# Performance work log

Measured on AMD Instinct MI355X. Metric: run time of the kernel, lower is better.

Reference implementation:

```python
import jax, jax.numpy as jnp
import numpy as np

MODEL_DIM = 1024
NUM_HEADS = 16
HEAD_DIM = MODEL_DIM // NUM_HEADS  # 64
MAX_SEQ = 1024
MAX_REL = 8


def setup_inputs() -> dict:
    key = jax.random.key(0)
    ks = jax.random.split(key, 5)
    B, S = 4, 1024
    x = jax.random.normal(ks[0], (B, S, MODEL_DIM), jnp.float32)
    W_in = jax.random.normal(ks[1], (MODEL_DIM, MODEL_DIM), jnp.float32) * 0.02
    W_out = jax.random.normal(ks[2], (MODEL_DIM, MODEL_DIM), jnp.float32) * 0.02
    # learned synthesized attention scores [1, H, max_seq, max_seq]
    attn_scores = jax.random.normal(ks[3], (1, NUM_HEADS, MAX_SEQ, MAX_SEQ), jnp.float32) * 0.05
    # relative-position VALUE embedding table [2*max_rel+1, head_dim]
    rel_values = jax.random.normal(ks[4], (2 * MAX_REL + 1, HEAD_DIM), jnp.float32) * 0.02
    return {"x": x, "W_in": W_in, "W_out": W_out,
            "attn_scores": attn_scores, "rel_values": rel_values}


def reference(x, W_in, W_out, attn_scores, rel_values):
    B, S, D = x.shape
    H, hd = NUM_HEADS, HEAD_DIM
    # in-projection (no bias), split heads: [B, H, S, hd]
    value = (x @ W_in.T).reshape(B, S, H, hd).transpose(0, 2, 1, 3)
    # learned (random-synthesizer) scores, sliced to seq len, broadcast over batch
    scores = attn_scores[:, :, :S, :S]              # [1, H, S, S]
    probs = jax.nn.softmax(scores, axis=-1)          # [1, H, S, S]
    probs = jnp.broadcast_to(probs, (B, H, S, S))
    # attention output: probs @ V
    out = jnp.einsum('bhsj,bhjd->bhsd', probs, value)  # [B, H, S, hd]
    # relative-position value contribution
    r = jnp.arange(S)
    dist = r[None, :] - r[:, None]                   # [S, S]
    idx = jnp.clip(dist, -MAX_REL, MAX_REL) + MAX_REL
    rel_emb = rel_values[idx]                        # [S, S, hd]
    out = out + jnp.einsum('bhsj,sjd->bhsd', probs, rel_emb)
    # join heads and out-project
    out = out.transpose(0, 2, 1, 3).reshape(B, S, H * hd)
    return out @ W_out.T                             # [B, S, D]
```

## Files before the change

kernel.cpp:

```cpp
#include <hip/hip_runtime.h>

typedef unsigned short ushort_t;
typedef __attribute__((ext_vector_type(4))) short short4_t;
typedef __attribute__((ext_vector_type(8))) short short8;
typedef __attribute__((ext_vector_type(4))) float floatx4;
typedef __attribute__((ext_vector_type(8))) __bf16 bf16x8;

__device__ __forceinline__ ushort_t f2b(float f) {
  union { float f; unsigned int i; } t; t.f = f;
  unsigned int u = t.i;
  return (ushort_t)((u + 0x7fffu + ((u >> 16) & 1u)) >> 16);
}

__device__ __forceinline__ floatx4 mfma16(short8 a, short8 b, floatx4 c) {
  return __builtin_amdgcn_mfma_f32_16x16x32_bf16(
      __builtin_bit_cast(bf16x8, a), __builtin_bit_cast(bf16x8, b), c, 0, 0, 0);
}

__device__ __forceinline__ void gload16(const void* g, void* l) {
  __builtin_amdgcn_global_load_lds(
      (const __attribute__((address_space(1))) void*)g,
      (__attribute__((address_space(3))) void*)l, 16, 0, 0);
}

__global__ __launch_bounds__(256) void k_f2b_all(
    const float* __restrict__ x, const float* __restrict__ Wi,
    const float* __restrict__ Wo, ushort_t* __restrict__ xb,
    ushort_t* __restrict__ Wib, ushort_t* __restrict__ Wob)
{
  const float* in; ushort_t* out; int i;
  if (blockIdx.x < 2048)      { in = x;  out = xb;  i = (blockIdx.x * 256 + threadIdx.x) * 8; }
  else if (blockIdx.x < 2560) { in = Wi; out = Wib; i = ((blockIdx.x - 2048) * 256 + threadIdx.x) * 8; }
  else                        { in = Wo; out = Wob; i = ((blockIdx.x - 2560) * 256 + threadIdx.x) * 8; }
  float4 a = *reinterpret_cast<const float4*>(in + i);
  float4 b = *reinterpret_cast<const float4*>(in + i + 4);
  short8 o;
  o[0] = (short)f2b(a.x); o[1] = (short)f2b(a.y);
  o[2] = (short)f2b(a.z); o[3] = (short)f2b(a.w);
  o[4] = (short)f2b(b.x); o[5] = (short)f2b(b.y);
  o[6] = (short)f2b(b.z); o[7] = (short)f2b(b.w);
  *reinterpret_cast<short8*>(out + i) = o;
}

__global__ __launch_bounds__(256) void k_softmax_rel(
    const float* __restrict__ S, const float* __restrict__ relv,
    ushort_t* __restrict__ P, float* __restrict__ R)
{
  __shared__ float mid[4][16];
  const int wave = threadIdx.x >> 6, lane = threadIdx.x & 63;
  const int row = blockIdx.x * 4 + wave;
  const int s = row & 1023;
  const float* src = S + (size_t)row * 1024;

  float v[4][4];
#pragma unroll
  for (int c = 0; c < 4; ++c) {
    float4 raw = *reinterpret_cast<const float4*>(src + c * 256 + lane * 4);
    v[c][0] = raw.x; v[c][1] = raw.y; v[c][2] = raw.z; v[c][3] = raw.w;
  }
  float m = -1e30f;
#pragma unroll
  for (int c = 0; c < 4; ++c)
#pragma unroll
    for (int e = 0; e < 4; ++e) m = fmaxf(m, v[c][e]);
#pragma unroll
  for (int d = 32; d; d >>= 1) m = fmaxf(m, __shfl_xor(m, d));

  float p[4][4];
  float tot = 0.f, sA = 0.f, sB = 0.f;
#pragma unroll
  for (int c = 0; c < 4; ++c) {
#pragma unroll
    for (int e = 0; e < 4; ++e) {
      int j = c * 256 + lane * 4 + e;
      float pe = __expf(v[c][e] - m);
      p[c][e] = pe;
      tot += pe;
      sA += (j <= s - 8) ? pe : 0.f;
      sB += (j >= s + 8) ? pe : 0.f;
    }
  }
#pragma unroll
  for (int d = 32; d; d >>= 1) {
    tot += __shfl_xor(tot, d);
    sA  += __shfl_xor(sA, d);
    sB  += __shfl_xor(sB, d);
  }
  const float inv = 1.0f / tot;

  if (lane < 16) mid[wave][lane] = 0.f;
  __syncthreads();
#pragma unroll
  for (int c = 0; c < 4; ++c) {
#pragma unroll
    for (int e = 0; e < 4; ++e) {
      int j = c * 256 + lane * 4 + e;
      int tt = j - (s - 7);
      if (tt >= 0 && tt < 15) mid[wave][tt] = p[c][e];
    }
  }
  __syncthreads();

  float acc = sA * relv[lane] + sB * relv[16 * 64 + lane];
#pragma unroll
  for (int tt = 0; tt < 15; ++tt)
    acc += mid[wave][tt] * relv[(1 + tt) * 64 + lane];
  R[(size_t)row * 64 + lane] = acc * inv;

#pragma unroll
  for (int c = 0; c < 4; ++c) {
    short4_t o;
#pragma unroll
    for (int e = 0; e < 4; ++e) o[e] = (short)f2b(p[c][e] * inv);
    *reinterpret_cast<short4_t*>(P + (size_t)row * 1024 + c * 256 + lane * 4) = o;
  }
}

__device__ __forceinline__ void gemm128_loop(
    const ushort_t* __restrict__ A0, const ushort_t* __restrict__ B0,
    ushort_t* sA, ushort_t* sB, floatx4 (&acc)[4][2])
{
  const int t = threadIdx.x;
  const int lane = t & 63, wave = t >> 6;
  const int wm = wave & 1, wn = wave >> 1;
  const int l15 = lane & 15, lk = lane >> 4;

#define STG(kt, buf)                                                        \
  {                                                                         \
    const int k0 = (kt) << 6;                                               \
    _Pragma("unroll")                                                       \
    for (int cc = 0; cc < 2; ++cc) {                                        \
      int c = t + (cc << 9);                                                \
      int r = c >> 3, cb = c & 7;                                           \
      int sc = k0 + ((cb ^ (r & 7)) << 3);                                  \
      gload16(A0 + (size_t)r * 1024 + sc, (char*)sA + (buf) * 16384 + c * 16); \
      gload16(B0 + (size_t)r * 1024 + sc, (char*)sB + (buf) * 16384 + c * 16); \
    }                                                                       \
  }

  STG(0, 0);
  STG(1, 1);
  for (int kt = 0; kt < 16; ++kt) {
    if (kt < 14) {
      STG(kt + 2, (kt + 2) & 3);
      asm volatile("s_waitcnt vmcnt(8)" ::: "memory");
    } else if (kt == 14) {
      asm volatile("s_waitcnt vmcnt(4)" ::: "memory");
    } else {
      asm volatile("s_waitcnt vmcnt(0)" ::: "memory");
    }
    __builtin_amdgcn_s_barrier();
    const char* bA = (const char*)sA + (kt & 3) * 16384;
    const char* bB = (const char*)sB + (kt & 3) * 16384;
#pragma unroll
    for (int kk = 0; kk < 2; ++kk) {
      const int cs = (kk << 2) + lk;
      short8 af[4], bf[2];
#pragma unroll
      for (int i = 0; i < 4; ++i) {
        int ra = (wm << 6) + (i << 4) + l15;
        af[i] = *reinterpret_cast<const short8*>(
            bA + ra * 128 + ((cs ^ (ra & 7)) << 4));
      }
#pragma unroll
      for (int j = 0; j < 2; ++j) {
        int rb = (wn << 5) + (j << 4) + l15;
        bf[j] = *reinterpret_cast<const short8*>(
            bB + rb * 128 + ((cs ^ (rb & 7)) << 4));
      }
      __builtin_amdgcn_s_setprio(1);
#pragma unroll
      for (int i = 0; i < 4; ++i)
#pragma unroll
        for (int j = 0; j < 2; ++j)
          acc[i][j] = mfma16(af[i], bf[j], acc[i][j]);
      __builtin_amdgcn_s_setprio(0);
    }
  }
#undef STG
}

__device__ __forceinline__ int xcd_swz(int bid) {
  return ((bid & 7) << 5) | (bid >> 3);
}

__global__ __launch_bounds__(512) void k_gemm_xw(
    const ushort_t* __restrict__ W, const ushort_t* __restrict__ X,
    ushort_t* __restrict__ Yt)
{
  __shared__ ushort_t sA[4 * 128 * 64];
  __shared__ ushort_t sB[4 * 128 * 64];
  const int lg = xcd_swz(blockIdx.x);
  const int m0 = (lg & 7) << 7, n0 = (lg >> 3) << 7;
  floatx4 acc[4][2] = {};
  gemm128_loop(W + (size_t)m0 * 1024, X + (size_t)n0 * 1024, sA, sB, acc);

  const int lane = threadIdx.x & 63, wave = threadIdx.x >> 6;
  const int wm = wave & 1, wn = wave >> 1;
  const int l15 = lane & 15, lk = lane >> 4;
#pragma unroll
  for (int i = 0; i < 4; ++i)
#pragma unroll
    for (int j = 0; j < 2; ++j)
#pragma unroll
      for (int rr = 0; rr < 4; ++rr) {
        int wrow = m0 + (wm << 6) + (i << 4) + (lk << 2) + rr;
        int col  = n0 + (wn << 5) + (j << 4) + l15;
        int h = wrow >> 6, d = wrow & 63;
        int b = col >> 10, s = col & 1023;
        Yt[(((size_t)((h << 2) + b) << 6) + d) * 1024 + s] = f2b(acc[i][j][rr]);
      }
}

__global__ __launch_bounds__(512) void k_head_pv(
    const ushort_t* __restrict__ P, const ushort_t* __restrict__ Yt,
    const float* __restrict__ R, ushort_t* __restrict__ O)
{
  __shared__ ushort_t sA[4 * 128 * 64];
  __shared__ ushort_t sB[4 * 128 * 64];
  const int lg = xcd_swz(blockIdx.x);
  const int h = lg >> 4, rem = lg & 15;
  const int m0 = (rem >> 1) << 7, n0 = (rem & 1) << 7;
  floatx4 acc[4][2] = {};
  gemm128_loop(P + ((size_t)h << 20) + (size_t)m0 * 1024,
               Yt + ((size_t)h << 18) + (size_t)n0 * 1024, sA, sB, acc);

  const int lane = threadIdx.x & 63, wave = threadIdx.x >> 6;
  const int wm = wave & 1, wn = wave >> 1;
  const int l15 = lane & 15, lk = lane >> 4;
#pragma unroll
  for (int i = 0; i < 4; ++i)
#pragma unroll
    for (int j = 0; j < 2; ++j)
#pragma unroll
      for (int rr = 0; rr < 4; ++rr) {
        int sr = m0 + (wm << 6) + (i << 4) + (lk << 2) + rr;
        int c  = n0 + (wn << 5) + (j << 4) + l15;
        int b = c >> 6, d = c & 63;
        float val = acc[i][j][rr] + R[(((size_t)h << 10) + sr) * 64 + d];
        O[((size_t)b << 20) + ((size_t)sr << 10) + (h << 6) + d] = f2b(val);
      }
}

__global__ __launch_bounds__(512) void k_gemm_out(
    const ushort_t* __restrict__ A, const ushort_t* __restrict__ B,
    float* __restrict__ C)
{
  __shared__ ushort_t sA[4 * 128 * 64];
  __shared__ ushort_t sB[4 * 128 * 64];
  const int lg = xcd_swz(blockIdx.x);
  const int m0 = (lg >> 3) << 7, n0 = (lg & 7) << 7;
  floatx4 acc[4][2] = {};
  gemm128_loop(A + (size_t)m0 * 1024, B + (size_t)n0 * 1024, sA, sB, acc);

  const int lane = threadIdx.x & 63, wave = threadIdx.x >> 6;
  const int wm = wave & 1, wn = wave >> 1;
  const int l15 = lane & 15, lk = lane >> 4;
#pragma unroll
  for (int i = 0; i < 4; ++i)
#pragma unroll
    for (int j = 0; j < 2; ++j)
#pragma unroll
      for (int rr = 0; rr < 4; ++rr) {
        int rowg = m0 + (wm << 6) + (i << 4) + (lk << 2) + rr;
        int colg = n0 + (wn << 5) + (j << 4) + l15;
        C[(size_t)rowg * 1024 + colg] = acc[i][j][rr];
      }
}

extern "C" void kernel_launch(void* const* d_in, const int* in_sizes, int n_in,
                              void* d_out, int out_size, void* d_ws, size_t ws_size,
                              hipStream_t stream)
{
  const float* x     = (const float*)d_in[0];
  const float* W_in  = (const float*)d_in[1];
  const float* W_out = (const float*)d_in[2];
  const float* attn  = (const float*)d_in[3];
  const float* relv  = (const float*)d_in[4];
  float* out = (float*)d_out;

  char* ws = (char*)d_ws;
  ushort_t* xb  = (ushort_t*)(ws);
  ushort_t* Wib = (ushort_t*)(ws + (8u << 20));
  ushort_t* Wob = (ushort_t*)(ws + (10u << 20));
  ushort_t* P   = (ushort_t*)(ws + (12u << 20));
  float*    R   = (float*)   (ws + (44u << 20));
  ushort_t* Yt  = (ushort_t*)(ws + (48u << 20));
  ushort_t* O   = (ushort_t*)(ws + (56u << 20));

  k_f2b_all<<<3072, 256, 0, stream>>>(x, W_in, W_out, xb, Wib, Wob);
  k_softmax_rel<<<4096, 256, 0, stream>>>(attn, relv, P, R);
  k_gemm_xw<<<256, 512, 0, stream>>>(Wib, xb, Yt);
  k_head_pv<<<256, 512, 0, stream>>>(P, Yt, R, O);
  k_gemm_out<<<256, 512, 0, stream>>>(O, Wob, out);
}
```

Before: 66.92 us.

## Merge softmax-rel and input-projection GEMM into one heterogeneous launch

Combines the independent softmax/relative-value kernel and the x·W_in GEMM into a single launch. The first 256 blocks do the GEMM and the remaining 2048 blocks each process 8 softmax rows, so the memory-bound softmax can overlap with the compute-bound GEMM and one launch is removed. To fit the shared 64KB buffer, the GEMM in this fused kernel drops from a 4-stage to a 2-stage, syncthreads-based pipeline, which may expose more load latency. The softmax blocks still allocate 64KB of LDS, which can limit how many run concurrently per CU.

```diff
diff --git a/kernel.cpp b/kernel.cpp
--- a/kernel.cpp
+++ b/kernel.cpp
@@ -42,107 +42,58 @@
   *reinterpret_cast<short8*>(out + i) = o;
 }
 
-__global__ __launch_bounds__(256) void k_softmax_rel(
-    const float* __restrict__ S, const float* __restrict__ relv,
-    ushort_t* __restrict__ P, float* __restrict__ R)
-{
-  __shared__ float mid[4][16];
-  const int wave = threadIdx.x >> 6, lane = threadIdx.x & 63;
-  const int row = blockIdx.x * 4 + wave;
-  const int s = row & 1023;
-  const float* src = S + (size_t)row * 1024;
-
-  float v[4][4];
-#pragma unroll
-  for (int c = 0; c < 4; ++c) {
-    float4 raw = *reinterpret_cast<const float4*>(src + c * 256 + lane * 4);
-    v[c][0] = raw.x; v[c][1] = raw.y; v[c][2] = raw.z; v[c][3] = raw.w;
-  }
-  float m = -1e30f;
-#pragma unroll
-  for (int c = 0; c < 4; ++c)
-#pragma unroll
-    for (int e = 0; e < 4; ++e) m = fmaxf(m, v[c][e]);
-#pragma unroll
-  for (int d = 32; d; d >>= 1) m = fmaxf(m, __shfl_xor(m, d));
-
-  float p[4][4];
-  float tot = 0.f, sA = 0.f, sB = 0.f;
-#pragma unroll
-  for (int c = 0; c < 4; ++c) {
-#pragma unroll
-    for (int e = 0; e < 4; ++e) {
-      int j = c * 256 + lane * 4 + e;
-      float pe = __expf(v[c][e] - m);
-      p[c][e] = pe;
-      tot += pe;
-      sA += (j <= s - 8) ? pe : 0.f;
-      sB += (j >= s + 8) ? pe : 0.f;
-    }
-  }
-#pragma unroll
-  for (int d = 32; d; d >>= 1) {
-    tot += __shfl_xor(tot, d);
-    sA  += __shfl_xor(sA, d);
-    sB  += __shfl_xor(sB, d);
-  }
-  const float inv = 1.0f / tot;
-
-  if (lane < 16) mid[wave][lane] = 0.f;
-  __syncthreads();
-#pragma unroll
-  for (int c = 0; c < 4; ++c) {
-#pragma unroll
-    for (int e = 0; e < 4; ++e) {
-      int j = c * 256 + lane * 4 + e;
-      int tt = j - (s - 7);
-      if (tt >= 0 && tt < 15) mid[wave][tt] = p[c][e];
-    }
-  }
-  __syncthreads();
-
-  float acc = sA * relv[lane] + sB * relv[16 * 64 + lane];
-#pragma unroll
-  for (int tt = 0; tt < 15; ++tt)
-    acc += mid[wave][tt] * relv[(1 + tt) * 64 + lane];
-  R[(size_t)row * 64 + lane] = acc * inv;
-
-#pragma unroll
-  for (int c = 0; c < 4; ++c) {
-    short4_t o;
-#pragma unroll
-    for (int e = 0; e < 4; ++e) o[e] = (short)f2b(p[c][e] * inv);
-    *reinterpret_cast<short4_t*>(P + (size_t)row * 1024 + c * 256 + lane * 4) = o;
-  }
-}
-
-__device__ __forceinline__ void gemm128_loop(
-    const ushort_t* __restrict__ A0, const ushort_t* __restrict__ B0,
-    ushort_t* sA, ushort_t* sB, floatx4 (&acc)[4][2])
-{
-  const int t = threadIdx.x;
-  const int lane = t & 63, wave = t >> 6;
-  const int wm = wave & 1, wn = wave >> 1;
-  const int l15 = lane & 15, lk = lane >> 4;
-
-#define STG(kt, buf)                                                        \
+#define STG(kt, buf, SLOTSZ)                                                \
   {                                                                         \
     const int k0 = (kt) << 6;                                               \
     _Pragma("unroll")                                                       \
     for (int cc = 0; cc < 2; ++cc) {                                        \
-      int c = t + (cc << 9);                                                \
+      int c = threadIdx.x + (cc << 9);                                      \
       int r = c >> 3, cb = c & 7;                                           \
       int sc = k0 + ((cb ^ (r & 7)) << 3);                                  \
-      gload16(A0 + (size_t)r * 1024 + sc, (char*)sA + (buf) * 16384 + c * 16); \
-      gload16(B0 + (size_t)r * 1024 + sc, (char*)sB + (buf) * 16384 + c * 16); \
+      gload16(A0 + (size_t)r * 1024 + sc, (char*)sA + (buf) * SLOTSZ + c * 16); \
+      gload16(B0 + (size_t)r * 1024 + sc, (char*)sB + (buf) * SLOTSZ + c * 16); \
     }                                                                       \
   }
 
-  STG(0, 0);
-  STG(1, 1);
+#define KSTEP_COMPUTE(bA, bB)                                               \
+  _Pragma("unroll")                                                         \
+  for (int kk = 0; kk < 2; ++kk) {                                          \
+    const int cs = (kk << 2) + lk;                                          \
+    short8 af[4], bf[2];                                                    \
+    _Pragma("unroll")                                                       \
+    for (int i = 0; i < 4; ++i) {                                           \
+      int ra = (wm << 6) + (i << 4) + l15;                                  \
+      af[i] = *reinterpret_cast<const short8*>(                             \
+          (bA) + ra * 128 + ((cs ^ (ra & 7)) << 4));                        \
+    }                                                                       \
+    _Pragma("unroll")                                                       \
+    for (int j = 0; j < 2; ++j) {                                           \
+      int rb = (wn << 5) + (j << 4) + l15;                                  \
+      bf[j] = *reinterpret_cast<const short8*>(                             \
+          (bB) + rb * 128 + ((cs ^ (rb & 7)) << 4));                        \
+    }                                                                       \
+    __builtin_amdgcn_s_setprio(1);                                          \
+    _Pragma("unroll")                                                       \
+    for (int i = 0; i < 4; ++i)                                             \
+      _Pragma("unroll")                                                     \
+      for (int j = 0; j < 2; ++j)                                           \
+        acc[i][j] = mfma16(af[i], bf[j], acc[i][j]);                        \
+    __builtin_amdgcn_s_setprio(0);                                          \
+  }
+
+__device__ __forceinline__ void gemm128_loop4(
+    const ushort_t* __restrict__ A0, const ushort_t* __restrict__ B0,
+    ushort_t* sA, ushort_t* sB, floatx4 (&acc)[4][2])
+{
+  const int lane = threadIdx.x & 63, wave = threadIdx.x >> 6;
+  const int wm = wave & 1, wn = wave >> 1;
+  const int l15 = lane & 15, lk = lane >> 4;
+
+  STG(0, 0, 16384);
+  STG(1, 1, 16384);
   for (int kt = 0; kt < 16; ++kt) {
     if (kt < 14) {
-      STG(kt + 2, (kt + 2) & 3);
+      STG(kt + 2, (kt + 2) & 3, 16384);
       asm volatile("s_waitcnt vmcnt(8)" ::: "memory");
     } else if (kt == 14) {
       asm volatile("s_waitcnt vmcnt(4)" ::: "memory");
@@ -152,64 +103,136 @@
     __builtin_amdgcn_s_barrier();
     const char* bA = (const char*)sA + (kt & 3) * 16384;
     const char* bB = (const char*)sB + (kt & 3) * 16384;
-#pragma unroll
-    for (int kk = 0; kk < 2; ++kk) {
-      const int cs = (kk << 2) + lk;
-      short8 af[4], bf[2];
-#pragma unroll
-      for (int i = 0; i < 4; ++i) {
-        int ra = (wm << 6) + (i << 4) + l15;
-        af[i] = *reinterpret_cast<const short8*>(
-            bA + ra * 128 + ((cs ^ (ra & 7)) << 4));
-      }
-#pragma unroll
-      for (int j = 0; j < 2; ++j) {
-        int rb = (wn << 5) + (j << 4) + l15;
-        bf[j] = *reinterpret_cast<const short8*>(
-            bB + rb * 128 + ((cs ^ (rb & 7)) << 4));
-      }
-      __builtin_amdgcn_s_setprio(1);
-#pragma unroll
-      for (int i = 0; i < 4; ++i)
-#pragma unroll
-        for (int j = 0; j < 2; ++j)
-          acc[i][j] = mfma16(af[i], bf[j], acc[i][j]);
-      __builtin_amdgcn_s_setprio(0);
-    }
-  }
-#undef STG
-}
-
-__device__ __forceinline__ int xcd_swz(int bid) {
-  return ((bid & 7) << 5) | (bid >> 3);
-}
-
-__global__ __launch_bounds__(512) void k_gemm_xw(
-    const ushort_t* __restrict__ W, const ushort_t* __restrict__ X,
-    ushort_t* __restrict__ Yt)
-{
-  __shared__ ushort_t sA[4 * 128 * 64];
-  __shared__ ushort_t sB[4 * 128 * 64];
-  const int lg = xcd_swz(blockIdx.x);
-  const int m0 = (lg & 7) << 7, n0 = (lg >> 3) << 7;
-  floatx4 acc[4][2] = {};
-  gemm128_loop(W + (size_t)m0 * 1024, X + (size_t)n0 * 1024, sA, sB, acc);
-
+    KSTEP_COMPUTE(bA, bB);
+  }
+}
+
+__device__ __forceinline__ void gemm128_loop2(
+    const ushort_t* __restrict__ A0, const ushort_t* __restrict__ B0,
+    ushort_t* sA, ushort_t* sB, floatx4 (&acc)[4][2])
+{
   const int lane = threadIdx.x & 63, wave = threadIdx.x >> 6;
   const int wm = wave & 1, wn = wave >> 1;
   const int l15 = lane & 15, lk = lane >> 4;
-#pragma unroll
-  for (int i = 0; i < 4; ++i)
-#pragma unroll
-    for (int j = 0; j < 2; ++j)
-#pragma unroll
-      for (int rr = 0; rr < 4; ++rr) {
-        int wrow = m0 + (wm << 6) + (i << 4) + (lk << 2) + rr;
-        int col  = n0 + (wn << 5) + (j << 4) + l15;
-        int h = wrow >> 6, d = wrow & 63;
-        int b = col >> 10, s = col & 1023;
-        Yt[(((size_t)((h << 2) + b) << 6) + d) * 1024 + s] = f2b(acc[i][j][rr]);
-      }
+
+  STG(0, 0, 16384);
+  for (int kt = 0; kt < 16; ++kt) {
+    __syncthreads();
+    if (kt < 15) STG(kt + 1, (kt + 1) & 1, 16384);
+    const char* bA = (const char*)sA + (kt & 1) * 16384;
+    const char* bB = (const char*)sB + (kt & 1) * 16384;
+    KSTEP_COMPUTE(bA, bB);
+  }
+}
+
+__device__ __forceinline__ int xcd_swz(int bid) {
+  return ((bid & 7) << 5) | (bid >> 3);
+}
+
+__global__ __launch_bounds__(512) void k_fused_sm_xw(
+    const float* __restrict__ S, const float* __restrict__ relv,
+    ushort_t* __restrict__ P, float* __restrict__ R,
+    const ushort_t* __restrict__ W, const ushort_t* __restrict__ X,
+    ushort_t* __restrict__ Yt)
+{
+  __shared__ __align__(16) char smem[65536];
+
+  if (blockIdx.x < 256) {
+    ushort_t* sA = (ushort_t*)smem;
+    ushort_t* sB = (ushort_t*)(smem + 32768);
+    const int lg = xcd_swz(blockIdx.x);
+    const int m0 = (lg & 7) << 7, n0 = (lg >> 3) << 7;
+    const ushort_t* A0 = W + (size_t)m0 * 1024;
+    const ushort_t* B0 = X + (size_t)n0 * 1024;
+    floatx4 acc[4][2] = {};
+    gemm128_loop2(A0, B0, sA, sB, acc);
+
+    const int lane = threadIdx.x & 63, wave = threadIdx.x >> 6;
+    const int wm = wave & 1, wn = wave >> 1;
+    const int l15 = lane & 15, lk = lane >> 4;
+#pragma unroll
+    for (int i = 0; i < 4; ++i)
+#pragma unroll
+      for (int j = 0; j < 2; ++j)
+#pragma unroll
+        for (int rr = 0; rr < 4; ++rr) {
+          int wrow = m0 + (wm << 6) + (i << 4) + (lk << 2) + rr;
+          int col  = n0 + (wn << 5) + (j << 4) + l15;
+          int h = wrow >> 6, d = wrow & 63;
+          int b = col >> 10, s = col & 1023;
+          Yt[(((size_t)((h << 2) + b) << 6) + d) * 1024 + s] = f2b(acc[i][j][rr]);
+        }
+    return;
+  }
+
+  float (*mid)[16] = (float (*)[16])smem;
+  const int wave = threadIdx.x >> 6, lane = threadIdx.x & 63;
+  const int row = (blockIdx.x - 256) * 8 + wave;
+  const int s = row & 1023;
+  const float* src = S + (size_t)row * 1024;
+
+  float v[4][4];
+#pragma unroll
+  for (int c = 0; c < 4; ++c) {
+    float4 raw = *reinterpret_cast<const float4*>(src + c * 256 + lane * 4);
+    v[c][0] = raw.x; v[c][1] = raw.y; v[c][2] = raw.z; v[c][3] = raw.w;
+  }
+  float m = -1e30f;
+#pragma unroll
+  for (int c = 0; c < 4; ++c)
+#pragma unroll
+    for (int e = 0; e < 4; ++e) m = fmaxf(m, v[c][e]);
+#pragma unroll
+  for (int d = 32; d; d >>= 1) m = fmaxf(m, __shfl_xor(m, d));
+
+  float p[4][4];
+  float tot = 0.f, sA = 0.f, sB = 0.f;
+#pragma unroll
+  for (int c = 0; c < 4; ++c) {
+#pragma unroll
+    for (int e = 0; e < 4; ++e) {
+      int j = c * 256 + lane * 4 + e;
+      float pe = __expf(v[c][e] - m);
+      p[c][e] = pe;
+      tot += pe;
+      sA += (j <= s - 8) ? pe : 0.f;
+      sB += (j >= s + 8) ? pe : 0.f;
+    }
+  }
+#pragma unroll
+  for (int d = 32; d; d >>= 1) {
+    tot += __shfl_xor(tot, d);
+    sA  += __shfl_xor(sA, d);
+    sB  += __shfl_xor(sB, d);
+  }
+  const float inv = 1.0f / tot;
+
+  if (lane < 16) mid[wave][lane] = 0.f;
+  __syncthreads();
+#pragma unroll
+  for (int c = 0; c < 4; ++c) {
+#pragma unroll
+    for (int e = 0; e < 4; ++e) {
+      int j = c * 256 + lane * 4 + e;
+      int tt = j - (s - 7);
+      if (tt >= 0 && tt < 15) mid[wave][tt] = p[c][e];
+    }
+  }
+  __syncthreads();
+
+  float acc = sA * relv[lane] + sB * relv[16 * 64 + lane];
+#pragma unroll
+  for (int tt = 0; tt < 15; ++tt)
+    acc += mid[wave][tt] * relv[(1 + tt) * 64 + lane];
+  R[(size_t)row * 64 + lane] = acc * inv;
+
+#pragma unroll
+  for (int c = 0; c < 4; ++c) {
+    short4_t o;
+#pragma unroll
+    for (int e = 0; e < 4; ++e) o[e] = (short)f2b(p[c][e] * inv);
+    *reinterpret_cast<short4_t*>(P + (size_t)row * 1024 + c * 256 + lane * 4) = o;
+  }
 }
 
 __global__ __launch_bounds__(512) void k_head_pv(
@@ -222,8 +245,8 @@
   const int h = lg >> 4, rem = lg & 15;
   const int m0 = (rem >> 1) << 7, n0 = (rem & 1) << 7;
   floatx4 acc[4][2] = {};
-  gemm128_loop(P + ((size_t)h << 20) + (size_t)m0 * 1024,
-               Yt + ((size_t)h << 18) + (size_t)n0 * 1024, sA, sB, acc);
+  gemm128_loop4(P + ((size_t)h << 20) + (size_t)m0 * 1024,
+                Yt + ((size_t)h << 18) + (size_t)n0 * 1024, sA, sB, acc);
 
   const int lane = threadIdx.x & 63, wave = threadIdx.x >> 6;
   const int wm = wave & 1, wn = wave >> 1;
@@ -251,7 +274,7 @@
   const int lg = xcd_swz(blockIdx.x);
   const int m0 = (lg >> 3) << 7, n0 = (lg & 7) << 7;
   floatx4 acc[4][2] = {};
-  gemm128_loop(A + (size_t)m0 * 1024, B + (size_t)n0 * 1024, sA, sB, acc);
+  gemm128_loop4(A + (size_t)m0 * 1024, B + (size_t)n0 * 1024, sA, sB, acc);
 
   const int lane = threadIdx.x & 63, wave = threadIdx.x >> 6;
   const int wm = wave & 1, wn = wave >> 1;
@@ -289,8 +312,7 @@
   ushort_t* O   = (ushort_t*)(ws + (56u << 20));
 
   k_f2b_all<<<3072, 256, 0, stream>>>(x, W_in, W_out, xb, Wib, Wob);
-  k_softmax_rel<<<4096, 256, 0, stream>>>(attn, relv, P, R);
-  k_gemm_xw<<<256, 512, 0, stream>>>(Wib, xb, Yt);
+  k_fused_sm_xw<<<2304, 512, 0, stream>>>(attn, relv, P, R, Wib, xb, Yt);
   k_head_pv<<<256, 512, 0, stream>>>(P, Yt, R, O);
   k_gemm_out<<<256, 512, 0, stream>>>(O, Wob, out);
 }
```

Measured after the change: 65.43 us. 2.2% less time.
